# Performance work log

Measured on AMD Instinct MI355X. Metric: run time of the kernel, lower is better.

## Reference

```python
import jax, jax.numpy as jnp
import numpy as np

D_HEAD = 64
SCALE = 1.0 / (D_HEAD ** 0.5)
MASK_VALUE = -1e9


def setup_inputs() -> dict:
    key = jax.random.key(0)
    kq, kk, kv, km = jax.random.split(key, 4)
    B, H, S, D = 2, 12, 2048, D_HEAD
    Q = jax.random.normal(kq, (B, H, S, D), dtype=jnp.float32)
    K = jax.random.normal(kk, (B, H, S, D), dtype=jnp.float32)
    V = jax.random.normal(kv, (B, H, S, D), dtype=jnp.float32)
    attn_mask = jax.random.randint(km, (B, 1, S, S), 0, 2).astype(bool)
    return {"Q": Q, "K": K, "V": V, "attn_mask": attn_mask}


def reference(Q, K, V, attn_mask):
    # scores: [B,H,S,S]
    scores = jnp.einsum('bhqd,bhkd->bhqk', Q, K) * SCALE
    scores = jnp.where(attn_mask, MASK_VALUE, scores)
    attn_prob = jax.nn.softmax(scores, axis=-1)
    # dropout p=0.0 (eval mode) -> identity
    context = jnp.einsum('bhqk,bhkd->bhqd', attn_prob, V)
    return (context, attn_prob)
```

## Files before the change

### kernel.cpp

```cpp
#include <hip/hip_runtime.h>
#include <hip/hip_bf16.h>
#include <math.h>

#define B_SZ   2
#define NH     12
#define S_LEN  2048
#define D_HD   64
#define NQ_EL  ((size_t)B_SZ * NH * S_LEN * D_HD)

typedef __attribute__((ext_vector_type(8))) __bf16 bf16x8;
typedef __attribute__((ext_vector_type(4))) __bf16 bf16x4;
typedef __attribute__((ext_vector_type(4))) float  f32x4;

__device__ __forceinline__ int detect_mask_mode64(const void* mask) {
  const int lane = threadIdx.x & 63;
  unsigned v = ((const unsigned*)mask)[lane];
  if (__ballot(v <= 1u) == ~0ull) return 0;
  if (__ballot(v == 0u || v == 0x3f800000u) == ~0ull) return 2;
  unsigned h0 = v & 0xFFFFu, h1 = v >> 16;
  bool okb = (h0 == 0u || h0 == 0x3f80u) && (h1 == 0u || h1 == 0x3f80u);
  if (__ballot(okb) == ~0ull) return 3;
  return 1;
}

__device__ __forceinline__ bool mask_at(const void* mask, int mode, size_t idx) {
  if (mode == 0) return ((const int*)mask)[idx] != 0;
  if (mode == 1) return ((const unsigned char*)mask)[idx] != 0;
  if (mode == 2) return ((const float*)mask)[idx] != 0.0f;
  return ((const unsigned short*)mask)[idx] != 0;
}

__global__ __launch_bounds__(256)
void build_bits_kernel(const void* __restrict__ mask, unsigned* __restrict__ bits) {
  const int mode = detect_mask_mode64(mask);
  const size_t i = (size_t)blockIdx.x * 256 + threadIdx.x;
  const bool m = mask_at(mask, mode, i);
  const unsigned long long bal = __ballot(m);
  const int lane = threadIdx.x & 63;
  if (lane == 0)       bits[i >> 5] = (unsigned)bal;
  else if (lane == 32) bits[i >> 5] = (unsigned)(bal >> 32);
}

__global__ __launch_bounds__(256)
void convert_kernel(const float* __restrict__ Q, const float* __restrict__ K,
                    const float* __restrict__ V,
                    __bf16* __restrict__ Qb, __bf16* __restrict__ Kb,
                    __bf16* __restrict__ Vb) {
  const size_t nvec = NQ_EL / 4;
  for (size_t vi = (size_t)blockIdx.x * 256 + threadIdx.x; vi < 3 * nvec;
       vi += (size_t)gridDim.x * 256) {
    const int seg = vi < nvec ? 0 : (vi < 2 * nvec ? 1 : 2);
    const size_t li = vi - (size_t)seg * nvec;
    const float* src = seg == 0 ? Q : (seg == 1 ? K : V);
    __bf16* dst = seg == 0 ? Qb : (seg == 1 ? Kb : Vb);
    const float scale = seg == 0 ? 0.125f : 1.0f;
    float4 a = ((const float4*)src)[li];
    __bf16 o0 = (__bf16)(a.x * scale), o1 = (__bf16)(a.y * scale);
    __bf16 o2 = (__bf16)(a.z * scale), o3 = (__bf16)(a.w * scale);
    ((ushort4*)dst)[li] = (ushort4){
        __builtin_bit_cast(unsigned short, o0), __builtin_bit_cast(unsigned short, o1),
        __builtin_bit_cast(unsigned short, o2), __builtin_bit_cast(unsigned short, o3)};
  }
}

__device__ __forceinline__ bf16x8 ld8s(const __bf16* p, float) {
  return *(const bf16x8*)p;
}
__device__ __forceinline__ bf16x8 ld8s(const float* p, float scale) {
  const float4 a = *(const float4*)p;
  const float4 b = *(const float4*)(p + 4);
  bf16x8 r;
  r[0] = (__bf16)(a.x * scale); r[1] = (__bf16)(a.y * scale);
  r[2] = (__bf16)(a.z * scale); r[3] = (__bf16)(a.w * scale);
  r[4] = (__bf16)(b.x * scale); r[5] = (__bf16)(b.y * scale);
  r[6] = (__bf16)(b.z * scale); r[7] = (__bf16)(b.w * scale);
  return r;
}

template<typename T, bool USE_BITS, bool PRESCALED>
__global__ __launch_bounds__(512)
void attn_kernel(const T* __restrict__ Qg, const T* __restrict__ Kg,
                 const T* __restrict__ Vg, const void* __restrict__ mask,
                 const unsigned* __restrict__ mbits, float* __restrict__ out_ctx)
{
  float* out_p = out_ctx + NQ_EL;

  const int flat = blockIdx.x + blockIdx.y * gridDim.x;
  const int wf   = (flat & 7) * 96 + (flat >> 3);
  const int qt   = wf & 31;
  const int bh   = wf >> 5;
  const int b    = bh / NH;

  const int tid  = threadIdx.x;
  const int lane = tid & 63;
  const int w    = tid >> 6;
  const int qw   = w & 3;
  const int kh   = w >> 2;
  const int qbase = qt * 64 + qw * 16;
  const int col  = lane & 15;
  const int g    = lane >> 4;
  const int q    = qbase + col;
  const int k0   = kh * (S_LEN / 2);

  int mmode = 0;
  if constexpr (!USE_BITS) mmode = detect_mask_mode64(mask);
  const size_t mrow  = (size_t)b * S_LEN * S_LEN;
  const size_t mbase = ((size_t)b * S_LEN + q) * (S_LEN / 32);

  const size_t qoff = ((size_t)bh * S_LEN + q) * D_HD + g * 8;
  const bf16x8 bq0 = ld8s(Qg + qoff,      PRESCALED ? 1.0f : 0.125f);
  const bf16x8 bq1 = ld8s(Qg + qoff + 32, PRESCALED ? 1.0f : 0.125f);

  float lsum = 0.f;
#pragma unroll 2
  for (int kc = k0; kc < k0 + S_LEN / 2; kc += 32) {
    unsigned mw = 0;
    if constexpr (USE_BITS) mw = mbits[mbase + (kc >> 5)];
#pragma unroll
    for (int sub = 0; sub < 2; ++sub) {
      const int kb = kc + sub * 16;
      const size_t koff = ((size_t)bh * S_LEN + kb + col) * D_HD + g * 8;
      bf16x8 ak0 = ld8s(Kg + koff,      1.0f);
      bf16x8 ak1 = ld8s(Kg + koff + 32, 1.0f);
      f32x4 acc = {0.f, 0.f, 0.f, 0.f};
      acc = __builtin_amdgcn_mfma_f32_16x16x32_bf16(ak0, bq0, acc, 0, 0, 0);
      acc = __builtin_amdgcn_mfma_f32_16x16x32_bf16(ak1, bq1, acc, 0, 0, 0);
#pragma unroll
      for (int r = 0; r < 4; ++r) {
        bool msk;
        if constexpr (USE_BITS) msk = (mw >> (sub * 16 + g * 4 + r)) & 1;
        else msk = mask_at(mask, mmode, mrow + (size_t)q * S_LEN + kb + g * 4 + r);
        lsum += msk ? 0.f : __expf(acc[r]);
      }
    }
  }
  lsum += __shfl_xor(lsum, 16);
  lsum += __shfl_xor(lsum, 32);

  __shared__ __align__(16) __bf16 vt[2][2][D_HD][36];
  __shared__ float lsh[8][16];
  __shared__ float csum[4][16][66];

  if (lane < 16) lsh[w][col] = lsum;

  auto stage = [&](int it_, int buf_) {
    const int kh2 = tid >> 8;
    const int rem = tid & 255;
    const int kk  = rem >> 3;
    const int d0  = (rem & 7) * 8;
    bf16x8 vv = ld8s(
        Vg + ((size_t)bh * S_LEN + kh2 * (S_LEN / 2) + it_ * 32 + kk) * D_HD + d0,
        1.0f);
#pragma unroll
    for (int j = 0; j < 8; j++) vt[buf_][kh2][d0 + j][kk] = vv[j];
  };
  stage(0, 0);
  __syncthreads();
  const float inv_l = 1.0f / (lsum + lsh[w ^ 4][col]);

  f32x4 cacc[4];
#pragma unroll
  for (int dt = 0; dt < 4; dt++) cacc[dt] = (f32x4){0.f, 0.f, 0.f, 0.f};

  float* prow = out_p + (size_t)bh * S_LEN * S_LEN + (size_t)q * S_LEN;

  for (int it = 0; it < S_LEN / 64; ++it) {
    const int cur = it & 1;
    if (it < 31) stage(it + 1, cur ^ 1);

    const int kc = k0 + it * 32;
    unsigned mw = 0;
    if constexpr (USE_BITS) mw = mbits[mbase + (kc >> 5)];

    float p[8];
#pragma unroll
    for (int sub = 0; sub < 2; ++sub) {
      const int kb = kc + sub * 16;
      const size_t koff = ((size_t)bh * S_LEN + kb + col) * D_HD + g * 8;
      bf16x8 ak0 = ld8s(Kg + koff,      1.0f);
      bf16x8 ak1 = ld8s(Kg + koff + 32, 1.0f);
      f32x4 acc = {0.f, 0.f, 0.f, 0.f};
      acc = __builtin_amdgcn_mfma_f32_16x16x32_bf16(ak0, bq0, acc, 0, 0, 0);
      acc = __builtin_amdgcn_mfma_f32_16x16x32_bf16(ak1, bq1, acc, 0, 0, 0);
#pragma unroll
      for (int r = 0; r < 4; ++r) {
        bool msk;
        if constexpr (USE_BITS) msk = (mw >> (sub * 16 + g * 4 + r)) & 1;
        else msk = mask_at(mask, mmode, mrow + (size_t)q * S_LEN + kb + g * 4 + r);
        p[sub * 4 + r] = msk ? 0.f : __expf(acc[r]) * inv_l;
      }
      float4 st = {p[sub * 4 + 0], p[sub * 4 + 1], p[sub * 4 + 2], p[sub * 4 + 3]};
      *(float4*)(prow + kb + g * 4) = st;
    }
    bf16x8 pa;
#pragma unroll
    for (int e = 0; e < 8; e++) pa[e] = (__bf16)p[e];

#pragma unroll
    for (int dt = 0; dt < 4; dt++) {
      const __bf16* vrow = &vt[cur][kh][dt * 16 + col][0];
      bf16x4 lo = *(const bf16x4*)(vrow + g * 4);
      bf16x4 hi = *(const bf16x4*)(vrow + 16 + g * 4);
      bf16x8 vf = __builtin_shufflevector(lo, hi, 0, 1, 2, 3, 4, 5, 6, 7);
      cacc[dt] = __builtin_amdgcn_mfma_f32_16x16x32_bf16(pa, vf, cacc[dt], 0, 0, 0);
    }
    __syncthreads();
  }

  if (kh == 1) {
#pragma unroll
    for (int dt = 0; dt < 4; dt++)
#pragma unroll
      for (int r = 0; r < 4; r++)
        csum[qw][g * 4 + r][dt * 16 + col] = cacc[dt][r];
  }
  __syncthreads();
  if (kh == 0) {
#pragma unroll
    for (int dt = 0; dt < 4; dt++)
#pragma unroll
      for (int r = 0; r < 4; r++)
        out_ctx[((size_t)bh * S_LEN + qbase + g * 4 + r) * D_HD + dt * 16 + col] =
            cacc[dt][r] + csum[qw][g * 4 + r][dt * 16 + col];
  }
}

extern "C" void kernel_launch(void* const* d_in, const int* in_sizes, int n_in,
                              void* d_out, int out_size, void* d_ws, size_t ws_size,
                              hipStream_t stream) {
  const float* Q = (const float*)d_in[0];
  const float* K = (const float*)d_in[1];
  const float* V = (const float*)d_in[2];
  const void* mask = d_in[3];
  float* out = (float*)d_out;

  const size_t mask_elems = (size_t)B_SZ * S_LEN * S_LEN;
  const size_t off_bits = 256;
  const size_t off_q = off_bits + mask_elems / 8;
  const size_t off_k = off_q + NQ_EL * 2;
  const size_t off_v = off_k + NQ_EL * 2;
  const size_t need  = off_v + NQ_EL * 2;
  dim3 grid(S_LEN / 64, B_SZ * NH);

  if (ws_size >= need) {
    unsigned* bits = (unsigned*)((char*)d_ws + off_bits);
    __bf16* Qb = (__bf16*)((char*)d_ws + off_q);
    __bf16* Kb = (__bf16*)((char*)d_ws + off_k);
    __bf16* Vb = (__bf16*)((char*)d_ws + off_v);
    build_bits_kernel<<<(unsigned)(mask_elems / 256), 256, 0, stream>>>(mask, bits);
    convert_kernel<<<2048, 256, 0, stream>>>(Q, K, V, Qb, Kb, Vb);
    attn_kernel<__bf16, true, true><<<grid, 512, 0, stream>>>(
        Qb, Kb, Vb, mask, bits, out);
  } else if (ws_size >= off_q) {
    unsigned* bits = (unsigned*)((char*)d_ws + off_bits);
    build_bits_kernel<<<(unsigned)(mask_elems / 256), 256, 0, stream>>>(mask, bits);
    attn_kernel<float, true, false><<<grid, 512, 0, stream>>>(
        Q, K, V, mask, bits, out);
  } else {
    attn_kernel<float, false, false><<<grid, 512, 0, stream>>>(
        Q, K, V, mask, nullptr, out);
  }
}
```

Measured before the change: 293.3 us.

## Fuse prep kernels and pre-transpose V to drop LDS staging in attention

Merges mask bit-packing and Q/K conversion into one prep kernel, which now also writes V transposed to bf16 [bh][d][k]. The main attention kernel then reads V fragments straight from global memory instead of staging them through shared memory with a per-iteration barrier. This removes one kernel launch and the __syncthreads in the inner loop. In exchange it relies on L2/cache hits for the 8-byte V reads, and the prep kernel does a shared-memory transpose.

```diff
diff --git a/kernel.cpp b/kernel.cpp
--- a/kernel.cpp
+++ b/kernel.cpp
@@ -31,42 +31,63 @@
 }
 
 __global__ __launch_bounds__(256)
-void build_bits_kernel(const void* __restrict__ mask, unsigned* __restrict__ bits) {
-  const int mode = detect_mask_mode64(mask);
-  const size_t i = (size_t)blockIdx.x * 256 + threadIdx.x;
-  const bool m = mask_at(mask, mode, i);
-  const unsigned long long bal = __ballot(m);
-  const int lane = threadIdx.x & 63;
-  if (lane == 0)       bits[i >> 5] = (unsigned)bal;
-  else if (lane == 32) bits[i >> 5] = (unsigned)(bal >> 32);
-}
-
-__global__ __launch_bounds__(256)
-void convert_kernel(const float* __restrict__ Q, const float* __restrict__ K,
-                    const float* __restrict__ V,
-                    __bf16* __restrict__ Qb, __bf16* __restrict__ Kb,
-                    __bf16* __restrict__ Vb) {
-  const size_t nvec = NQ_EL / 4;
-  for (size_t vi = (size_t)blockIdx.x * 256 + threadIdx.x; vi < 3 * nvec;
-       vi += (size_t)gridDim.x * 256) {
-    const int seg = vi < nvec ? 0 : (vi < 2 * nvec ? 1 : 2);
-    const size_t li = vi - (size_t)seg * nvec;
-    const float* src = seg == 0 ? Q : (seg == 1 ? K : V);
-    __bf16* dst = seg == 0 ? Qb : (seg == 1 ? Kb : Vb);
-    const float scale = seg == 0 ? 0.125f : 1.0f;
-    float4 a = ((const float4*)src)[li];
-    __bf16 o0 = (__bf16)(a.x * scale), o1 = (__bf16)(a.y * scale);
-    __bf16 o2 = (__bf16)(a.z * scale), o3 = (__bf16)(a.w * scale);
-    ((ushort4*)dst)[li] = (ushort4){
-        __builtin_bit_cast(unsigned short, o0), __builtin_bit_cast(unsigned short, o1),
-        __builtin_bit_cast(unsigned short, o2), __builtin_bit_cast(unsigned short, o3)};
-  }
-}
-
-__device__ __forceinline__ bf16x8 ld8s(const __bf16* p, float) {
-  return *(const bf16x8*)p;
-}
-__device__ __forceinline__ bf16x8 ld8s(const float* p, float scale) {
+void prep_kernel(const float* __restrict__ Q, const float* __restrict__ K,
+                 const float* __restrict__ V, const void* __restrict__ mask,
+                 unsigned* __restrict__ bits, __bf16* __restrict__ Qb,
+                 __bf16* __restrict__ Kb, __bf16* __restrict__ VT) {
+  const int blk = blockIdx.x;
+  const int tid = threadIdx.x;
+  if (blk < 512) {
+    const int mode = detect_mask_mode64(mask);
+    const int lane = tid & 63;
+#pragma unroll 4
+    for (int i = 0; i < 64; ++i) {
+      const size_t idx = ((size_t)blk * 64 + i) * 256 + tid;
+      const unsigned long long bal = __ballot(mask_at(mask, mode, idx));
+      if (lane == 0)       bits[idx >> 5] = (unsigned)bal;
+      else if (lane == 32) bits[idx >> 5] = (unsigned)(bal >> 32);
+    }
+  } else if (blk < 1536) {
+    const bool isq = blk < 1024;
+    const float* src = isq ? Q : K;
+    __bf16* dst = isq ? Qb : Kb;
+    const float scale = isq ? 0.125f : 1.0f;
+    const size_t base = (size_t)(blk & 511) * 256 + tid;
+#pragma unroll
+    for (int i = 0; i < 6; ++i) {
+      const size_t li = base + (size_t)i * 512 * 256;
+      float4 a = ((const float4*)src)[li];
+      __bf16 o0 = (__bf16)(a.x * scale), o1 = (__bf16)(a.y * scale);
+      __bf16 o2 = (__bf16)(a.z * scale), o3 = (__bf16)(a.w * scale);
+      ((ushort4*)dst)[li] = (ushort4){
+          __builtin_bit_cast(unsigned short, o0), __builtin_bit_cast(unsigned short, o1),
+          __builtin_bit_cast(unsigned short, o2), __builtin_bit_cast(unsigned short, o3)};
+    }
+  } else {
+    __shared__ __align__(16) __bf16 tl[D_HD][72];
+    const int t  = blk - 1536;
+    const int bh = t >> 5;
+    const int k0 = (t & 31) * 64;
+#pragma unroll
+    for (int i = 0; i < 4; ++i) {
+      const int vi = i * 256 + tid;
+      const int kk = vi >> 4, dv = (vi & 15) * 4;
+      float4 f = *(const float4*)(V + ((size_t)bh * S_LEN + k0 + kk) * D_HD + dv);
+      tl[dv + 0][kk] = (__bf16)f.x; tl[dv + 1][kk] = (__bf16)f.y;
+      tl[dv + 2][kk] = (__bf16)f.z; tl[dv + 3][kk] = (__bf16)f.w;
+    }
+    __syncthreads();
+#pragma unroll
+    for (int half = 0; half < 2; ++half) {
+      const int d = half * 32 + (tid >> 3);
+      const int kc = (tid & 7) * 8;
+      bf16x8 vv = *(const bf16x8*)&tl[d][kc];
+      *(bf16x8*)(VT + ((size_t)bh * D_HD + d) * S_LEN + k0 + kc) = vv;
+    }
+  }
+}
+
+__device__ __forceinline__ bf16x8 ld8f(const float* p, float scale) {
   const float4 a = *(const float4*)p;
   const float4 b = *(const float4*)(p + 4);
   bf16x8 r;
@@ -77,11 +98,10 @@
   return r;
 }
 
-template<typename T, bool USE_BITS, bool PRESCALED>
 __global__ __launch_bounds__(512)
-void attn_kernel(const T* __restrict__ Qg, const T* __restrict__ Kg,
-                 const T* __restrict__ Vg, const void* __restrict__ mask,
-                 const unsigned* __restrict__ mbits, float* __restrict__ out_ctx)
+void attn_main(const __bf16* __restrict__ Qb, const __bf16* __restrict__ Kb,
+               const __bf16* __restrict__ VT, const unsigned* __restrict__ mbits,
+               float* __restrict__ out_ctx)
 {
   float* out_p = out_ctx + NQ_EL;
 
@@ -101,18 +121,127 @@
   const int g    = lane >> 4;
   const int q    = qbase + col;
   const int k0   = kh * (S_LEN / 2);
-
+  const size_t mbase = ((size_t)b * S_LEN + q) * (S_LEN / 32);
+
+  const size_t qoff = ((size_t)bh * S_LEN + q) * D_HD + g * 8;
+  const bf16x8 bq0 = *(const bf16x8*)(Qb + qoff);
+  const bf16x8 bq1 = *(const bf16x8*)(Qb + qoff + 32);
+
+  float lsum = 0.f;
+#pragma unroll 2
+  for (int kc = k0; kc < k0 + S_LEN / 2; kc += 32) {
+    const unsigned mw = mbits[mbase + (kc >> 5)];
+#pragma unroll
+    for (int sub = 0; sub < 2; ++sub) {
+      const int kb = kc + sub * 16;
+      const size_t koff = ((size_t)bh * S_LEN + kb + col) * D_HD + g * 8;
+      bf16x8 ak0 = *(const bf16x8*)(Kb + koff);
+      bf16x8 ak1 = *(const bf16x8*)(Kb + koff + 32);
+      f32x4 acc = {0.f, 0.f, 0.f, 0.f};
+      acc = __builtin_amdgcn_mfma_f32_16x16x32_bf16(ak0, bq0, acc, 0, 0, 0);
+      acc = __builtin_amdgcn_mfma_f32_16x16x32_bf16(ak1, bq1, acc, 0, 0, 0);
+#pragma unroll
+      for (int r = 0; r < 4; ++r) {
+        const bool msk = (mw >> (sub * 16 + g * 4 + r)) & 1;
+        lsum += msk ? 0.f : __expf(acc[r]);
+      }
+    }
+  }
+  lsum += __shfl_xor(lsum, 16);
+  lsum += __shfl_xor(lsum, 32);
+
+  __shared__ float lsh[8][16];
+  __shared__ float csum[4][16][66];
+  if (lane < 16) lsh[w][col] = lsum;
+  __syncthreads();
+  const float inv_l = 1.0f / (lsum + lsh[w ^ 4][col]);
+
+  f32x4 cacc[4];
+#pragma unroll
+  for (int dt = 0; dt < 4; dt++) cacc[dt] = (f32x4){0.f, 0.f, 0.f, 0.f};
+
+  float* prow = out_p + (size_t)bh * S_LEN * S_LEN + (size_t)q * S_LEN;
+  const __bf16* vbase = VT + (size_t)bh * D_HD * S_LEN;
+
+  for (int it = 0; it < S_LEN / 64; ++it) {
+    const int kc = k0 + it * 32;
+    const unsigned mw = mbits[mbase + (kc >> 5)];
+
+    float p[8];
+#pragma unroll
+    for (int sub = 0; sub < 2; ++sub) {
+      const int kb = kc + sub * 16;
+      const size_t koff = ((size_t)bh * S_LEN + kb + col) * D_HD + g * 8;
+      bf16x8 ak0 = *(const bf16x8*)(Kb + koff);
+      bf16x8 ak1 = *(const bf16x8*)(Kb + koff + 32);
+      f32x4 acc = {0.f, 0.f, 0.f, 0.f};
+      acc = __builtin_amdgcn_mfma_f32_16x16x32_bf16(ak0, bq0, acc, 0, 0, 0);
+      acc = __builtin_amdgcn_mfma_f32_16x16x32_bf16(ak1, bq1, acc, 0, 0, 0);
+#pragma unroll
+      for (int r = 0; r < 4; ++r) {
+        const bool msk = (mw >> (sub * 16 + g * 4 + r)) & 1;
+        p[sub * 4 + r] = msk ? 0.f : __expf(acc[r]) * inv_l;
+      }
+      float4 st = {p[sub * 4 + 0], p[sub * 4 + 1], p[sub * 4 + 2], p[sub * 4 + 3]};
+      *(float4*)(prow + kb + g * 4) = st;
+    }
+    bf16x8 pa;
+#pragma unroll
+    for (int e = 0; e < 8; e++) pa[e] = (__bf16)p[e];
+
+#pragma unroll
+    for (int dt = 0; dt < 4; dt++) {
+      const __bf16* vrow = vbase + (size_t)(dt * 16 + col) * S_LEN + kc;
+      bf16x4 lo = *(const bf16x4*)(vrow + g * 4);
+      bf16x4 hi = *(const bf16x4*)(vrow + 16 + g * 4);
+      bf16x8 vf = __builtin_shufflevector(lo, hi, 0, 1, 2, 3, 4, 5, 6, 7);
+      cacc[dt] = __builtin_amdgcn_mfma_f32_16x16x32_bf16(pa, vf, cacc[dt], 0, 0, 0);
+    }
+  }
+
+  if (kh == 1) {
+#pragma unroll
+    for (int dt = 0; dt < 4; dt++)
+#pragma unroll
+      for (int r = 0; r < 4; r++)
+        csum[qw][g * 4 + r][dt * 16 + col] = cacc[dt][r];
+  }
+  __syncthreads();
+  if (kh == 0) {
+#pragma unroll
+    for (int dt = 0; dt < 4; dt++)
+#pragma unroll
+      for (int r = 0; r < 4; r++)
+        out_ctx[((size_t)bh * S_LEN + qbase + g * 4 + r) * D_HD + dt * 16 + col] =
+            cacc[dt][r] + csum[qw][g * 4 + r][dt * 16 + col];
+  }
+}
+
+template<bool USE_BITS>
+__global__ __launch_bounds__(512)
+void attn_fb(const float* __restrict__ Qg, const float* __restrict__ Kg,
+             const float* __restrict__ Vg, const void* __restrict__ mask,
+             const unsigned* __restrict__ mbits, float* __restrict__ out_ctx)
+{
+  float* out_p = out_ctx + NQ_EL;
+  const int flat = blockIdx.x + blockIdx.y * gridDim.x;
+  const int wf   = (flat & 7) * 96 + (flat >> 3);
+  const int qt = wf & 31, bh = wf >> 5, b = bh / NH;
+  const int tid = threadIdx.x, lane = tid & 63, w = tid >> 6;
+  const int qw = w & 3, kh = w >> 2;
+  const int qbase = qt * 64 + qw * 16;
+  const int col = lane & 15, g = lane >> 4;
+  const int q = qbase + col;
+  const int k0 = kh * (S_LEN / 2);
   int mmode = 0;
   if constexpr (!USE_BITS) mmode = detect_mask_mode64(mask);
   const size_t mrow  = (size_t)b * S_LEN * S_LEN;
   const size_t mbase = ((size_t)b * S_LEN + q) * (S_LEN / 32);
-
   const size_t qoff = ((size_t)bh * S_LEN + q) * D_HD + g * 8;
-  const bf16x8 bq0 = ld8s(Qg + qoff,      PRESCALED ? 1.0f : 0.125f);
-  const bf16x8 bq1 = ld8s(Qg + qoff + 32, PRESCALED ? 1.0f : 0.125f);
+  const bf16x8 bq0 = ld8f(Qg + qoff, 0.125f);
+  const bf16x8 bq1 = ld8f(Qg + qoff + 32, 0.125f);
 
   float lsum = 0.f;
-#pragma unroll 2
   for (int kc = k0; kc < k0 + S_LEN / 2; kc += 32) {
     unsigned mw = 0;
     if constexpr (USE_BITS) mw = mbits[mbase + (kc >> 5)];
@@ -120,8 +249,8 @@
     for (int sub = 0; sub < 2; ++sub) {
       const int kb = kc + sub * 16;
       const size_t koff = ((size_t)bh * S_LEN + kb + col) * D_HD + g * 8;
-      bf16x8 ak0 = ld8s(Kg + koff,      1.0f);
-      bf16x8 ak1 = ld8s(Kg + koff + 32, 1.0f);
+      bf16x8 ak0 = ld8f(Kg + koff, 1.0f);
+      bf16x8 ak1 = ld8f(Kg + koff + 32, 1.0f);
       f32x4 acc = {0.f, 0.f, 0.f, 0.f};
       acc = __builtin_amdgcn_mfma_f32_16x16x32_bf16(ak0, bq0, acc, 0, 0, 0);
       acc = __builtin_amdgcn_mfma_f32_16x16x32_bf16(ak1, bq1, acc, 0, 0, 0);
@@ -136,49 +265,28 @@
   }
   lsum += __shfl_xor(lsum, 16);
   lsum += __shfl_xor(lsum, 32);
-
-  __shared__ __align__(16) __bf16 vt[2][2][D_HD][36];
   __shared__ float lsh[8][16];
   __shared__ float csum[4][16][66];
-
   if (lane < 16) lsh[w][col] = lsum;
-
-  auto stage = [&](int it_, int buf_) {
-    const int kh2 = tid >> 8;
-    const int rem = tid & 255;
-    const int kk  = rem >> 3;
-    const int d0  = (rem & 7) * 8;
-    bf16x8 vv = ld8s(
-        Vg + ((size_t)bh * S_LEN + kh2 * (S_LEN / 2) + it_ * 32 + kk) * D_HD + d0,
-        1.0f);
-#pragma unroll
-    for (int j = 0; j < 8; j++) vt[buf_][kh2][d0 + j][kk] = vv[j];
-  };
-  stage(0, 0);
   __syncthreads();
   const float inv_l = 1.0f / (lsum + lsh[w ^ 4][col]);
 
   f32x4 cacc[4];
 #pragma unroll
   for (int dt = 0; dt < 4; dt++) cacc[dt] = (f32x4){0.f, 0.f, 0.f, 0.f};
-
   float* prow = out_p + (size_t)bh * S_LEN * S_LEN + (size_t)q * S_LEN;
 
   for (int it = 0; it < S_LEN / 64; ++it) {
-    const int cur = it & 1;
-    if (it < 31) stage(it + 1, cur ^ 1);
-
     const int kc = k0 + it * 32;
     unsigned mw = 0;
     if constexpr (USE_BITS) mw = mbits[mbase + (kc >> 5)];
-
     float p[8];
 #pragma unroll
     for (int sub = 0; sub < 2; ++sub) {
       const int kb = kc + sub * 16;
       const size_t koff = ((size_t)bh * S_LEN + kb + col) * D_HD + g * 8;
-      bf16x8 ak0 = ld8s(Kg + koff,      1.0f);
-      bf16x8 ak1 = ld8s(Kg + koff + 32, 1.0f);
+      bf16x8 ak0 = ld8f(Kg + koff, 1.0f);
+      bf16x8 ak1 = ld8f(Kg + koff + 32, 1.0f);
       f32x4 acc = {0.f, 0.f, 0.f, 0.f};
       acc = __builtin_amdgcn_mfma_f32_16x16x32_bf16(ak0, bq0, acc, 0, 0, 0);
       acc = __builtin_amdgcn_mfma_f32_16x16x32_bf16(ak1, bq1, acc, 0, 0, 0);
@@ -195,18 +303,17 @@
     bf16x8 pa;
 #pragma unroll
     for (int e = 0; e < 8; e++) pa[e] = (__bf16)p[e];
-
 #pragma unroll
     for (int dt = 0; dt < 4; dt++) {
-      const __bf16* vrow = &vt[cur][kh][dt * 16 + col][0];
-      bf16x4 lo = *(const bf16x4*)(vrow + g * 4);
-      bf16x4 hi = *(const bf16x4*)(vrow + 16 + g * 4);
-      bf16x8 vf = __builtin_shufflevector(lo, hi, 0, 1, 2, 3, 4, 5, 6, 7);
+      bf16x8 vf;
+#pragma unroll
+      for (int e = 0; e < 8; e++) {
+        const int kidx = kc + (e >> 2) * 16 + g * 4 + (e & 3);
+        vf[e] = (__bf16)Vg[((size_t)bh * S_LEN + kidx) * D_HD + dt * 16 + col];
+      }
       cacc[dt] = __builtin_amdgcn_mfma_f32_16x16x32_bf16(pa, vf, cacc[dt], 0, 0, 0);
     }
-    __syncthreads();
-  }
-
+  }
   if (kh == 1) {
 #pragma unroll
     for (int dt = 0; dt < 4; dt++)
@@ -223,6 +330,16 @@
         out_ctx[((size_t)bh * S_LEN + qbase + g * 4 + r) * D_HD + dt * 16 + col] =
             cacc[dt][r] + csum[qw][g * 4 + r][dt * 16 + col];
   }
+}
+
+__global__ __launch_bounds__(256)
+void build_bits_kernel(const void* __restrict__ mask, unsigned* __restrict__ bits) {
+  const int mode = detect_mask_mode64(mask);
+  const size_t i = (size_t)blockIdx.x * 256 + threadIdx.x;
+  const unsigned long long bal = __ballot(mask_at(mask, mode, i));
+  const int lane = threadIdx.x & 63;
+  if (lane == 0)       bits[i >> 5] = (unsigned)bal;
+  else if (lane == 32) bits[i >> 5] = (unsigned)(bal >> 32);
 }
 
 extern "C" void kernel_launch(void* const* d_in, const int* in_sizes, int n_in,
@@ -236,28 +353,24 @@
 
   const size_t mask_elems = (size_t)B_SZ * S_LEN * S_LEN;
   const size_t off_bits = 256;
-  const size_t off_q = off_bits + mask_elems / 8;
-  const size_t off_k = off_q + NQ_EL * 2;
-  const size_t off_v = off_k + NQ_EL * 2;
-  const size_t need  = off_v + NQ_EL * 2;
+  const size_t off_q  = off_bits + mask_elems / 8;
+  const size_t off_k  = off_q + NQ_EL * 2;
+  const size_t off_vt = off_k + NQ_EL * 2;
+  const size_t need   = off_vt + NQ_EL * 2;
   dim3 grid(S_LEN / 64, B_SZ * NH);
 
   if (ws_size >= need) {
     unsigned* bits = (unsigned*)((char*)d_ws + off_bits);
     __bf16* Qb = (__bf16*)((char*)d_ws + off_q);
     __bf16* Kb = (__bf16*)((char*)d_ws + off_k);
-    __bf16* Vb = (__bf16*)((char*)d_ws + off_v);
-    build_bits_kernel<<<(unsigned)(mask_elems / 256), 256, 0, stream>>>(mask, bits);
-    convert_kernel<<<2048, 256, 0, stream>>>(Q, K, V, Qb, Kb, Vb);
-    attn_kernel<__bf16, true, true><<<grid, 512, 0, stream>>>(
-        Qb, Kb, Vb, mask, bits, out);
+    __bf16* VT = (__bf16*)((char*)d_ws + off_vt);
+    prep_kernel<<<2304, 256, 0, stream>>>(Q, K, V, mask, bits, Qb, Kb, VT);
+    attn_main<<<grid, 512, 0, stream>>>(Qb, Kb, VT, bits, out);
   } else if (ws_size >= off_q) {
     unsigned* bits = (unsigned*)((char*)d_ws + off_bits);
     build_bits_kernel<<<(unsigned)(mask_elems / 256), 256, 0, stream>>>(mask, bits);
-    attn_kernel<float, true, false><<<grid, 512, 0, stream>>>(
-        Q, K, V, mask, bits, out);
+    attn_fb<true><<<grid, 512, 0, stream>>>(Q, K, V, mask, bits, out);
   } else {
-    attn_kernel<float, false, false><<<grid, 512, 0, stream>>>(
-        Q, K, V, mask, nullptr, out);
-  }
-}
+    attn_fb<false><<<grid, 512, 0, stream>>>(Q, K, V, mask, nullptr, out);
+  }
+}
```

New measurement: 438.0 us. +49.3%, slower.
